# Kernel optimization log

Hardware: AMD Instinct MI355X
Metric: run time of the kernel (lower is better)

The kernel has to match this reference:

```python
import jax, jax.numpy as jnp
import numpy as np

D = 4096
H = 4 * D
EPS = 1e-5


def layer_norm(x, g, b):
    mu = jnp.mean(x, axis=-1, keepdims=True)
    var = jnp.mean(jnp.square(x - mu), axis=-1, keepdims=True)
    return (x - mu) * jax.lax.rsqrt(var + EPS) * g + b


def setup_inputs() -> dict:
    key = jax.random.key(0)
    ks = jax.random.split(key, 8)
    s = 0.02
    return {
        "x": jax.random.normal(ks[0], (2, 2048, D), dtype=jnp.float32),
        "Wq": jax.random.normal(ks[1], (D, D), dtype=jnp.float32) * s,
        "bq": jnp.zeros((D,), jnp.float32),
        "Wk": jax.random.normal(ks[2], (D, D), dtype=jnp.float32) * s,
        "bk": jnp.zeros((D,), jnp.float32),
        "Wv": jax.random.normal(ks[3], (D, D), dtype=jnp.float32) * s,
        "bv": jnp.zeros((D,), jnp.float32),
        "Wo": jax.random.normal(ks[4], (D, D), dtype=jnp.float32) * s,
        "bo": jnp.zeros((D,), jnp.float32),
        "g1": jnp.ones((D,), jnp.float32),
        "b1": jnp.zeros((D,), jnp.float32),
        "g2": jnp.ones((D,), jnp.float32),
        "b2": jnp.zeros((D,), jnp.float32),
        "W1": jax.random.normal(ks[5], (D, H), dtype=jnp.float32) * s,
        "bi1": jnp.zeros((H,), jnp.float32),
        "W2": jax.random.normal(ks[6], (H, D), dtype=jnp.float32) * s,
        "bi2": jnp.zeros((D,), jnp.float32),
    }


def reference(x, Wq, bq, Wk, bk, Wv, bv, Wo, bo, g1, b1, g2, b2, W1, bi1, W2, bi2):
    # single-head attention, scale = sqrt(D) (as in the source)
    Q = x @ Wq + bq          # [B, S, D]
    K = x @ Wk + bk
    V = x @ Wv + bv
    scores = jnp.einsum("bsd,btd->bst", Q, K) / jnp.sqrt(jnp.float32(D))
    attn = jax.nn.softmax(scores, axis=-1) @ V   # [B, S, D]
    x = attn @ Wo + bo + x
    x = layer_norm(x, g1, b1)
    h = jax.nn.gelu(x @ W1 + bi1, approximate=False)  # torch nn.GELU default = exact erf
    x = h @ W2 + bi2 + x
    x = layer_norm(x, g2, b2)
    return x
```

## Files before the change

kernel.cpp:

```cpp
#include <hip/hip_runtime.h>
#include <hip/hip_bf16.h>

typedef __bf16 bf16x8 __attribute__((ext_vector_type(8)));
typedef float  f32x4  __attribute__((ext_vector_type(4)));
typedef unsigned short u16;
typedef unsigned int   u32;

#define DEV __device__ __forceinline__

DEV u16 f2bu(float f){ union{float f; u32 i;} x; x.f=f; u32 r=x.i+0x7FFFu+((x.i>>16)&1u); return (u16)(r>>16); }
DEV u32 pack2(float a, float b){ return (u32)f2bu(a) | ((u32)f2bu(b)<<16); }

DEV void gload16(const u16* g, u16* l){
  __builtin_amdgcn_global_load_lds((const __attribute__((address_space(1))) void*)g,
                                   (__attribute__((address_space(3))) void*)l, 16, 0, 0);
}

template<int BIAS, int GELU, int RESF32, int OUTF32>
DEV void gemm_body(
    const u16* __restrict__ A, const u16* __restrict__ Bt,
    const float* __restrict__ bias, const float* __restrict__ resid,
    float* __restrict__ outF, u16* __restrict__ outB,
    int M, int N, int K, int SWZ,
    long long sA, long long sB, long long sC)
{
  __shared__ __align__(16) u16 As[4][8192];
  __shared__ __align__(16) u16 Bs[4][8192];

  const int tid  = threadIdx.x;
  const int lane = tid & 63;
  const int wave = tid >> 6;
  const int wm = wave >> 2;
  const int wn = wave & 3;

  int bx = blockIdx.x, by = blockIdx.y;
  if (SWZ) {
    const int gx = gridDim.x, gy = gridDim.y;
    const int f  = by * gx + bx;
    const int S  = gy << 4;
    const int s  = f / S;
    const int r  = f - s * S;
    bx = (s << 4) + (r & 15);
    by = r >> 4;
  }
  const int rowBase = by * 256;
  const int colBase = bx * 256;

  const u16* Ag = A + (size_t)blockIdx.z * sA + (size_t)rowBase * K;
  const u16* Bg = Bt + (size_t)blockIdx.z * sB + (size_t)colBase * K;

  const int qsw = (lane & 3) ^ ((lane >> 3) & 3);
  const u16* apA0 = Ag + (size_t)(wave*32 + (lane>>2)) * K + qsw*8;
  const u16* apA1 = apA0 + (size_t)16 * K;
  const u16* apB0 = Bg + (size_t)(wave*32 + (lane>>2)) * K + qsw*8;
  const u16* apB1 = apB0 + (size_t)16 * K;
  u16* dA0 = &As[0][wave*1024 + lane*8];
  u16* dA1 = dA0 + 512;
  u16* dB0 = &Bs[0][wave*1024 + lane*8];
  u16* dB1 = dB0 + 512;

#define STAGE(t) { const int _b = (t) & 3; const size_t _k = (size_t)(t) * 32;          \
    gload16(apA0 + _k, dA0 + _b*8192); gload16(apA1 + _k, dA1 + _b*8192);               \
    gload16(apB0 + _k, dB0 + _b*8192); gload16(apB1 + _k, dB1 + _b*8192); }

  const int r15 = lane & 15;
  const int gp  = (lane >> 4) ^ ((lane >> 1) & 3);
  const u16* rdA = &As[0][(wm*128 + r15)*32 + gp*8];
  const u16* rdB = &Bs[0][(wn*64  + r15)*32 + gp*8];

  f32x4 acc[8][4];
  const f32x4 fz = {0.f,0.f,0.f,0.f};
#pragma unroll
  for (int m=0;m<8;++m)
#pragma unroll
    for (int n=0;n<4;++n) acc[m][n] = fz;

  const int KT = K >> 5;
  STAGE(0);
  if (KT > 1) STAGE(1);
  if (KT > 2) STAGE(2);

  for (int t = 0; t < KT; ++t) {
    const int rem = KT - t;
    if (rem > 2)      asm volatile("s_waitcnt vmcnt(8)" ::: "memory");
    else if (rem > 1) asm volatile("s_waitcnt vmcnt(4)" ::: "memory");
    else              asm volatile("s_waitcnt vmcnt(0)" ::: "memory");
    __builtin_amdgcn_s_barrier();
    asm volatile("" ::: "memory");

    const u16* pa = rdA + (t & 3) * 8192;
    const u16* pb = rdB + (t & 3) * 8192;
    bf16x8 a[8], b[4];
#pragma unroll
    for (int m=0;m<8;++m) a[m] = *(const bf16x8*)(pa + m*512);
#pragma unroll
    for (int n=0;n<4;++n) b[n] = *(const bf16x8*)(pb + n*512);

    if (t + 3 < KT) STAGE(t + 3);

    __builtin_amdgcn_s_setprio(1);
#pragma unroll
    for (int m=0;m<8;++m)
#pragma unroll
      for (int n=0;n<4;++n)
        acc[m][n] = __builtin_amdgcn_mfma_f32_16x16x32_bf16(a[m], b[n], acc[m][n], 0,0,0);
    __builtin_amdgcn_s_setprio(0);
  }
#undef STAGE

  const long long cb = (long long)blockIdx.z * sC;
  const int q4 = (lane >> 4) * 4;
#pragma unroll
  for (int m=0;m<8;++m){
    const int row0 = rowBase + wm*128 + m*16 + q4;
#pragma unroll
    for (int n=0;n<4;++n){
      const int col = colBase + wn*64 + n*16 + r15;
      float bb = 0.f;
      if (BIAS) bb = bias[col];
#pragma unroll
      for (int r=0;r<4;++r){
        float v = acc[m][n][r] + bb;
        if (GELU) v = 0.5f*v*(1.f+erff(v*0.70710678118654752f));
        const size_t oi = (size_t)cb + (size_t)(row0+r)*N + col;
        if (RESF32) v += resid[oi];
        if (OUTF32) outF[oi] = v;
        else        outB[oi] = f2bu(v);
      }
    }
  }
}

#define GEMM_KERNEL(NAME, BIAS, GELU, RESF32, OUTF32)                      \
__global__ __launch_bounds__(512, 2) void NAME(                           \
    const u16* __restrict__ A, const u16* __restrict__ Bt,                 \
    const float* __restrict__ bias, const float* __restrict__ resid,       \
    float* __restrict__ outF, u16* __restrict__ outB,                      \
    int M, int N, int K, int SWZ,                                          \
    long long sA, long long sB, long long sC) {                            \
  gemm_body<BIAS,GELU,RESF32,OUTF32>(A,Bt,bias,resid,outF,outB,M,N,K,SWZ,sA,sB,sC); }

GEMM_KERNEL(gemm_q,   1,0,0,0)
GEMM_KERNEL(gemm_k,   1,0,0,0)
GEMM_KERNEL(gemm_v,   1,0,0,0)
GEMM_KERNEL(gemm_qkt, 0,0,0,1)
GEMM_KERNEL(gemm_pv,  0,0,0,0)
GEMM_KERNEL(gemm_o,   1,0,1,1)
GEMM_KERNEL(gemm_f1,  1,1,0,0)
GEMM_KERNEL(gemm_f2,  1,0,1,1)

__global__ __launch_bounds__(256) void tr_f32_bf16(
    const float* __restrict__ in, u16* __restrict__ out, int R, int C)
{
  __shared__ float tile[64][65];
  const int t = threadIdx.x;
  const int tr = blockIdx.y*64, tc = blockIdx.x*64;
  const int c4 = (t&15)*4;
#pragma unroll
  for (int i=0;i<4;++i){
    const int r = i*16 + (t>>4);
    const float4 v = *reinterpret_cast<const float4*>(&in[(size_t)(tr+r)*C + tc + c4]);
    tile[r][c4+0]=v.x; tile[r][c4+1]=v.y; tile[r][c4+2]=v.z; tile[r][c4+3]=v.w;
  }
  __syncthreads();
#pragma unroll
  for (int i=0;i<4;++i){
    const int c = i*16 + (t>>4);
    uint2 o;
    o.x = pack2(tile[c4+0][c], tile[c4+1][c]);
    o.y = pack2(tile[c4+2][c], tile[c4+3][c]);
    *reinterpret_cast<uint2*>(&out[(size_t)(tc+c)*R + tr + c4]) = o;
  }
}

__global__ __launch_bounds__(256) void tr_bf16(
    const u16* __restrict__ in, u16* __restrict__ out, int R, int C,
    long long sIn, long long sOut)
{
  __shared__ u16 tile[64][72];
  const long long z = blockIdx.z;
  in  += z*sIn; out += z*sOut;
  const int t = threadIdx.x;
  const int tr = blockIdx.y*64, tc = blockIdx.x*64;
  const int c4 = (t&15)*4;
#pragma unroll
  for (int i=0;i<4;++i){
    const int r = i*16 + (t>>4);
    const uint2 v = *reinterpret_cast<const uint2*>(&in[(size_t)(tr+r)*C + tc + c4]);
    tile[r][c4+0]=(u16)(v.x&0xffffu); tile[r][c4+1]=(u16)(v.x>>16);
    tile[r][c4+2]=(u16)(v.y&0xffffu); tile[r][c4+3]=(u16)(v.y>>16);
  }
  __syncthreads();
#pragma unroll
  for (int i=0;i<4;++i){
    const int c = i*16 + (t>>4);
    uint2 o;
    o.x = (u32)tile[c4+0][c] | ((u32)tile[c4+1][c]<<16);
    o.y = (u32)tile[c4+2][c] | ((u32)tile[c4+3][c]<<16);
    *reinterpret_cast<uint2*>(&out[(size_t)(tc+c)*R + tr + c4]) = o;
  }
}

__global__ __launch_bounds__(256) void cvt_f32_bf16(
    const float* __restrict__ in, u16* __restrict__ out, int n4)
{
  const int i = blockIdx.x*256 + threadIdx.x;
  if (i >= n4) return;
  const float4 v = reinterpret_cast<const float4*>(in)[i];
  uint2 o; o.x = pack2(v.x,v.y); o.y = pack2(v.z,v.w);
  reinterpret_cast<uint2*>(out)[i] = o;
}

__global__ __launch_bounds__(256) void softmax2048(
    const float* __restrict__ S, u16* __restrict__ P, float scale)
{
  const size_t row = blockIdx.x;
  const float4* src = reinterpret_cast<const float4*>(S + row*2048);
  const int t = threadIdx.x, lane = t&63, wave = t>>6;
  const float4 a = src[t], b = src[t+256];
  float v[8] = {a.x,a.y,a.z,a.w,b.x,b.y,b.z,b.w};
  float m = -3.4e38f;
#pragma unroll
  for (int i=0;i<8;++i){ v[i]*=scale; m = fmaxf(m, v[i]); }
#pragma unroll
  for (int o=32;o>0;o>>=1) m = fmaxf(m, __shfl_xor(m, o));
  __shared__ float red[8];
  if (lane==0) red[wave]=m;
  __syncthreads();
  m = fmaxf(fmaxf(red[0],red[1]), fmaxf(red[2],red[3]));
  float s = 0.f;
#pragma unroll
  for (int i=0;i<8;++i){ v[i] = __expf(v[i]-m); s += v[i]; }
#pragma unroll
  for (int o=32;o>0;o>>=1) s += __shfl_xor(s, o);
  if (lane==0) red[4+wave]=s;
  __syncthreads();
  s = red[4]+red[5]+red[6]+red[7];
  const float r = 1.f/s;
  uint2 o1, o2;
  o1.x = pack2(v[0]*r, v[1]*r); o1.y = pack2(v[2]*r, v[3]*r);
  o2.x = pack2(v[4]*r, v[5]*r); o2.y = pack2(v[6]*r, v[7]*r);
  uint2* dst = reinterpret_cast<uint2*>(P + row*2048);
  dst[t] = o1; dst[t+256] = o2;
}

template<int WB>
__global__ __launch_bounds__(256) void layernorm4096(
    const float* __restrict__ X, const float* __restrict__ g,
    const float* __restrict__ b, float* __restrict__ Yf, u16* __restrict__ Yb)
{
  const size_t row = blockIdx.x;
  const float4* src = reinterpret_cast<const float4*>(X + row*4096);
  const int t = threadIdx.x, lane = t&63, wave = t>>6;
  float4 xv[4];
  float sum=0.f, ss=0.f;
#pragma unroll
  for (int i=0;i<4;++i){
    xv[i] = src[t + 256*i];
    sum += xv[i].x+xv[i].y+xv[i].z+xv[i].w;
    ss  += xv[i].x*xv[i].x + xv[i].y*xv[i].y + xv[i].z*xv[i].z + xv[i].w*xv[i].w;
  }
#pragma unroll
  for (int o=32;o>0;o>>=1){ sum += __shfl_xor(sum,o); ss += __shfl_xor(ss,o); }
  __shared__ float rs[4], rq[4];
  if (lane==0){ rs[wave]=sum; rq[wave]=ss; }
  __syncthreads();
  sum = rs[0]+rs[1]+rs[2]+rs[3];
  ss  = rq[0]+rq[1]+rq[2]+rq[3];
  const float mean = sum * (1.f/4096.f);
  const float var  = ss * (1.f/4096.f) - mean*mean;
  const float rstd = rsqrtf(var + 1e-5f);
#pragma unroll
  for (int i=0;i<4;++i){
    const int i4 = t + 256*i;
    const float4 gv = reinterpret_cast<const float4*>(g)[i4];
    const float4 bvv = reinterpret_cast<const float4*>(b)[i4];
    float4 y;
    y.x = (xv[i].x-mean)*rstd*gv.x + bvv.x;
    y.y = (xv[i].y-mean)*rstd*gv.y + bvv.y;
    y.z = (xv[i].z-mean)*rstd*gv.z + bvv.z;
    y.w = (xv[i].w-mean)*rstd*gv.w + bvv.w;
    reinterpret_cast<float4*>(Yf + row*4096)[i4] = y;
    if (WB){
      uint2 o; o.x = pack2(y.x,y.y); o.y = pack2(y.z,y.w);
      reinterpret_cast<uint2*>(Yb + row*4096)[i4] = o;
    }
  }
}

extern "C" void kernel_launch(void* const* d_in, const int* in_sizes, int n_in,
                              void* d_out, int out_size, void* d_ws, size_t ws_size,
                              hipStream_t stream)
{
  constexpr int D = 4096, HD = 16384, S = 2048, B = 2;
  constexpr int NT = B*S;
  const float* x   = (const float*)d_in[0];
  const float* Wq  = (const float*)d_in[1];
  const float* bq  = (const float*)d_in[2];
  const float* Wk  = (const float*)d_in[3];
  const float* bk  = (const float*)d_in[4];
  const float* Wv  = (const float*)d_in[5];
  const float* bvp = (const float*)d_in[6];
  const float* Wo  = (const float*)d_in[7];
  const float* bo  = (const float*)d_in[8];
  const float* g1  = (const float*)d_in[9];
  const float* b1  = (const float*)d_in[10];
  const float* g2  = (const float*)d_in[11];
  const float* b2  = (const float*)d_in[12];
  const float* W1  = (const float*)d_in[13];
  const float* bi1 = (const float*)d_in[14];
  const float* W2  = (const float*)d_in[15];
  const float* bi2 = (const float*)d_in[16];

  char* ws = (char*)d_ws;
  const size_t MB32 = 33554432;
  u16* WqT = (u16*)(ws + 0*MB32);
  u16* WkT = (u16*)(ws + 1*MB32);
  u16* WvT = (u16*)(ws + 2*MB32);
  u16* WoT = (u16*)(ws + 3*MB32);
  u16* W1T = (u16*)(ws + 0*MB32);
  u16* xb  = (u16*)(ws + 4*MB32);
  u16* Qb  = (u16*)(ws + 5*MB32);
  u16* Kb  = (u16*)(ws + 6*MB32);
  u16* Vb  = (u16*)(ws + 7*MB32);
  u16* W2T = (u16*)(ws + 4*MB32);
  u16* Vt  = (u16*)(ws + 8*MB32);
  float* scoresF = (float*)(ws + 9*MB32);
  u16* Pb  = (u16*)(ws + 10*MB32);
  u16* Ab  = (u16*)(ws + 10*MB32 + 16777216);
  u16* hB  = (u16*)(ws + 8*MB32);
  float* x1raw = (float*)(ws + 12*MB32);
  float* x2raw = (float*)(ws + 12*MB32);
  float* x1f   = (float*)(ws + 14*MB32);
  u16*   x1b   = (u16*)(ws + 16*MB32);

  const dim3 blk(256), blkG(512);
  const long long SD = (long long)S*D, SS = (long long)S*S, DS = (long long)D*S;

  tr_f32_bf16<<<dim3(D/64, D/64), blk, 0, stream>>>(Wq, WqT, D, D);
  tr_f32_bf16<<<dim3(D/64, D/64), blk, 0, stream>>>(Wk, WkT, D, D);
  tr_f32_bf16<<<dim3(D/64, D/64), blk, 0, stream>>>(Wv, WvT, D, D);
  tr_f32_bf16<<<dim3(D/64, D/64), blk, 0, stream>>>(Wo, WoT, D, D);
  cvt_f32_bf16<<<dim3((NT*D/4)/256), blk, 0, stream>>>(x, xb, NT*D/4);

  gemm_q<<<dim3(D/256, NT/256, 1), blkG, 0, stream>>>(xb, WqT, bq,  nullptr, nullptr, Qb, NT, D, D, 1, 0,0,0);
  gemm_k<<<dim3(D/256, NT/256, 1), blkG, 0, stream>>>(xb, WkT, bk,  nullptr, nullptr, Kb, NT, D, D, 1, 0,0,0);
  gemm_v<<<dim3(D/256, NT/256, 1), blkG, 0, stream>>>(xb, WvT, bvp, nullptr, nullptr, Vb, NT, D, D, 1, 0,0,0);
  tr_bf16<<<dim3(D/64, S/64, B), blk, 0, stream>>>(Vb, Vt, S, D, SD, SD);

  gemm_qkt<<<dim3(S/256, S/256, B), blkG, 0, stream>>>(Qb, Kb, nullptr, nullptr, scoresF, nullptr, S, S, D, 0, SD, SD, SS);
  softmax2048<<<dim3(B*S), blk, 0, stream>>>(scoresF, Pb, 0.015625f);
  gemm_pv<<<dim3(D/256, S/256, B), blkG, 0, stream>>>(Pb, Vt, nullptr, nullptr, nullptr, Ab, S, D, S, 0, SS, DS, SD);

  gemm_o<<<dim3(D/256, NT/256, 1), blkG, 0, stream>>>(Ab, WoT, bo, x, x1raw, nullptr, NT, D, D, 1, 0,0,0);
  layernorm4096<1><<<dim3(NT), blk, 0, stream>>>(x1raw, g1, b1, x1f, x1b);

  tr_f32_bf16<<<dim3(HD/64, D/64), blk, 0, stream>>>(W1, W1T, D, HD);
  gemm_f1<<<dim3(HD/256, NT/256, 1), blkG, 0, stream>>>(x1b, W1T, bi1, nullptr, nullptr, hB, NT, HD, D, 1, 0,0,0);
  tr_f32_bf16<<<dim3(D/64, HD/64), blk, 0, stream>>>(W2, W2T, HD, D);
  gemm_f2<<<dim3(D/256, NT/256, 1), blkG, 0, stream>>>(hB, W2T, bi2, x1f, x2raw, nullptr, NT, D, HD, 1, 0,0,0);
  layernorm4096<0><<<dim3(NT), blk, 0, stream>>>(x2raw, g2, b2, (float*)d_out, nullptr);
}
```

Before: 2.205 ms.

## Split GEMM main loop into two half-tile phases with interleaved staging

Restructures the 256x256 bf16 GEMM k-loop into two phases. Each phase loads half of the A fragments, issues half of the next global-to-LDS stage (A or B), and runs 16 MFMAs, with barriers placed between phases to stagger waves, in the style of a ping-pong schedule. The intent is to overlap LDS reads and global load issue with MFMA work and to lower register pressure by holding only four A fragments at a time. In exchange it doubles the number of barriers per iteration and makes vmcnt bookkeeping more intricate.

```diff
diff --git a/kernel.cpp b/kernel.cpp
--- a/kernel.cpp
+++ b/kernel.cpp
@@ -59,8 +59,9 @@
   u16* dB0 = &Bs[0][wave*1024 + lane*8];
   u16* dB1 = dB0 + 512;
 
-#define STAGE(t) { const int _b = (t) & 3; const size_t _k = (size_t)(t) * 32;          \
-    gload16(apA0 + _k, dA0 + _b*8192); gload16(apA1 + _k, dA1 + _b*8192);               \
+#define STAGE_A(t) { const int _b = (t) & 3; const size_t _k = (size_t)(t) * 32;        \
+    gload16(apA0 + _k, dA0 + _b*8192); gload16(apA1 + _k, dA1 + _b*8192); }
+#define STAGE_B(t) { const int _b = (t) & 3; const size_t _k = (size_t)(t) * 32;        \
     gload16(apB0 + _k, dB0 + _b*8192); gload16(apB1 + _k, dB1 + _b*8192); }
 
   const int r15 = lane & 15;
@@ -76,37 +77,59 @@
     for (int n=0;n<4;++n) acc[m][n] = fz;
 
   const int KT = K >> 5;
-  STAGE(0);
-  if (KT > 1) STAGE(1);
-  if (KT > 2) STAGE(2);
+  STAGE_A(0); STAGE_B(0);
+  if (KT > 1) { STAGE_A(1); STAGE_B(1); }
+  if (KT > 2) { STAGE_A(2); STAGE_B(2); }
+  if (KT > 2)      asm volatile("s_waitcnt vmcnt(8)" ::: "memory");
+  else if (KT > 1) asm volatile("s_waitcnt vmcnt(4)" ::: "memory");
+  else             asm volatile("s_waitcnt vmcnt(0)" ::: "memory");
+  __builtin_amdgcn_s_barrier();
+  asm volatile("" ::: "memory");
 
   for (int t = 0; t < KT; ++t) {
-    const int rem = KT - t;
-    if (rem > 2)      asm volatile("s_waitcnt vmcnt(8)" ::: "memory");
-    else if (rem > 1) asm volatile("s_waitcnt vmcnt(4)" ::: "memory");
-    else              asm volatile("s_waitcnt vmcnt(0)" ::: "memory");
-    __builtin_amdgcn_s_barrier();
-    asm volatile("" ::: "memory");
-
     const u16* pa = rdA + (t & 3) * 8192;
     const u16* pb = rdB + (t & 3) * 8192;
-    bf16x8 a[8], b[4];
-#pragma unroll
-    for (int m=0;m<8;++m) a[m] = *(const bf16x8*)(pa + m*512);
-#pragma unroll
-    for (int n=0;n<4;++n) b[n] = *(const bf16x8*)(pb + n*512);
-
-    if (t + 3 < KT) STAGE(t + 3);
-
+    bf16x8 a0[4], a1[4], b[4];
+
+#pragma unroll
+    for (int i=0;i<4;++i) a0[i] = *(const bf16x8*)(pa + i*512);
+#pragma unroll
+    for (int i=0;i<4;++i) b[i]  = *(const bf16x8*)(pb + i*512);
+    if (t + 3 < KT) STAGE_A(t + 3);
+    asm volatile("" ::: "memory");
+    __builtin_amdgcn_s_barrier();
+    asm volatile("s_waitcnt lgkmcnt(0)" ::: "memory");
     __builtin_amdgcn_s_setprio(1);
 #pragma unroll
-    for (int m=0;m<8;++m)
+    for (int m=0;m<4;++m)
 #pragma unroll
       for (int n=0;n<4;++n)
-        acc[m][n] = __builtin_amdgcn_mfma_f32_16x16x32_bf16(a[m], b[n], acc[m][n], 0,0,0);
+        acc[m][n] = __builtin_amdgcn_mfma_f32_16x16x32_bf16(a0[m], b[n], acc[m][n], 0,0,0);
     __builtin_amdgcn_s_setprio(0);
-  }
-#undef STAGE
+    asm volatile("" ::: "memory");
+    __builtin_amdgcn_s_barrier();
+
+#pragma unroll
+    for (int i=0;i<4;++i) a1[i] = *(const bf16x8*)(pa + (i+4)*512);
+    if (t + 3 < KT) STAGE_B(t + 3);
+    if (t + 3 < KT)      asm volatile("s_waitcnt vmcnt(8)" ::: "memory");
+    else if (t + 2 < KT) asm volatile("s_waitcnt vmcnt(4)" ::: "memory");
+    else if (t + 1 < KT) asm volatile("s_waitcnt vmcnt(0)" ::: "memory");
+    asm volatile("" ::: "memory");
+    __builtin_amdgcn_s_barrier();
+    asm volatile("s_waitcnt lgkmcnt(0)" ::: "memory");
+    __builtin_amdgcn_s_setprio(1);
+#pragma unroll
+    for (int m=0;m<4;++m)
+#pragma unroll
+      for (int n=0;n<4;++n)
+        acc[m+4][n] = __builtin_amdgcn_mfma_f32_16x16x32_bf16(a1[m], b[n], acc[m+4][n], 0,0,0);
+    __builtin_amdgcn_s_setprio(0);
+    asm volatile("" ::: "memory");
+    __builtin_amdgcn_s_barrier();
+  }
+#undef STAGE_A
+#undef STAGE_B
 
   const long long cb = (long long)blockIdx.z * sC;
   const int q4 = (lane >> 4) * 4;
```

After: 2.402 ms. 8.9% more time.
